# Optimization experiments

Measured on AMD Instinct MI355X. Metric: run time of the kernel, lower is better.

The kernel has to match this reference:

```python
import jax, jax.numpy as jnp
import numpy as np
import math

B, C, SEG, SEGLEN, K, GROUPS, WG = 8, 256, 40, 200, 10, 32, 4
L4 = SEGLEN // 4            # 50 temporal slots per segment
N = SEG * L4                # 2000 total points
WIDTH = GROUPS * WG         # 128 bottleneck width


def build_neighbor_idx(seg_lens):
    """Exact numpy replication of torch get_temporal_graph's neighbor-list loop.
    Returns flat (into B*N rows) neighbor indices of shape (B, N, 3)."""
    seg_lens = np.asarray(seg_lens)
    Bn, S = seg_lens.shape
    nb = np.zeros((Bn, S * L4, 3), dtype=np.int64)
    for i in range(Bn):
        last_valid = 0
        skip_seg = 0
        base = i * S * L4
        for j in range(S):
            valid = math.ceil(seg_lens[i, j] / 4.0)
            for k in range(L4):
                idx = j * L4 + k
                if k < valid:
                    nb[i, idx] = [base + last_valid, base + idx, base + idx]
                    last_valid = idx
                    if k == 0 and j != 0:
                        nb[i, skip_seg, 2] = base + idx
                    if k == valid - 1:
                        skip_seg = idx
                    else:
                        nb[i, idx, 2] = base + idx + 1
                else:
                    nb[i, idx] = [base + idx] * 3
    return nb


def conv1x1(x, W, b):
    # x: (B, Cin, N, T), W: (Cout, Cin)
    return jnp.einsum('bcnt,oc->bont', x, W) + b[None, :, None, None]


def grouped_1x3(x, W, b):
    # x: (B, WIDTH, N, 3), W: (WIDTH, WIDTH//GROUPS, 3); valid conv -> T_out = 1
    Bn, _, Nn, _ = x.shape
    xg = x.reshape(Bn, GROUPS, WIDTH // GROUPS, Nn, 3)
    Wg = W.reshape(GROUPS, WIDTH // GROUPS, WIDTH // GROUPS, 3)
    y = jnp.einsum('bgcnt,goct->bgon', xg, Wg)
    return y.reshape(Bn, WIDTH, Nn, 1) + b[None, :, None, None]


def grouped_1x1(x, W, b):
    # x: (B, WIDTH, N, T), W: (WIDTH, WIDTH//GROUPS)
    Bn, _, Nn, T = x.shape
    xg = x.reshape(Bn, GROUPS, WIDTH // GROUPS, Nn, T)
    Wg = W.reshape(GROUPS, WIDTH // GROUPS, WIDTH // GROUPS)
    y = jnp.einsum('bgcnt,goc->bgont', xg, Wg)
    return y.reshape(Bn, WIDTH, Nn, T) + b[None, :, None, None]


def setup_inputs() -> dict:
    key = jax.random.key(0)
    ks = jax.random.split(key, 10)
    s = 0.05
    x = jax.random.normal(ks[0], (B, C, N), dtype=jnp.float32)
    seg_lens = jax.random.randint(ks[1], (B, SEG), 0, 201)
    neighbor_idx = jnp.asarray(build_neighbor_idx(np.asarray(seg_lens)))
    return dict(
        x=x, seg_lens=seg_lens, neighbor_idx=neighbor_idx,
        tW1=jax.random.normal(ks[2], (WIDTH, C), jnp.float32) * s,
        tb1=jnp.zeros((WIDTH,), jnp.float32),
        tW2=jax.random.normal(ks[3], (WIDTH, WIDTH // GROUPS, 3), jnp.float32) * s,
        tb2=jnp.zeros((WIDTH,), jnp.float32),
        tW3=jax.random.normal(ks[4], (C, WIDTH), jnp.float32) * s,
        tb3=jnp.zeros((C,), jnp.float32),
        sW1=jax.random.normal(ks[5], (WIDTH, 2 * C), jnp.float32) * s,
        sb1=jnp.zeros((WIDTH,), jnp.float32),
        sW2=jax.random.normal(ks[6], (WIDTH, WIDTH // GROUPS), jnp.float32) * s,
        sb2=jnp.zeros((WIDTH,), jnp.float32),
        sW3=jax.random.normal(ks[7], (C, WIDTH), jnp.float32) * s,
        sb3=jnp.zeros((C,), jnp.float32),
    )


def reference(x, seg_lens, neighbor_idx, tW1, tb1, tW2, tb2, tW3, tb3,
              sW1, sb1, sW2, sb2, sW3, sb3):
    relu = jax.nn.relu
    B_, C_, N_ = x.shape
    flat = x.transpose(0, 2, 1).reshape(B_ * N_, C_)  # (B*N, C)

    # --- temporal branch: gather 3 temporal-graph neighbors -> (B, C, N, 3) ---
    tg = flat[neighbor_idx.reshape(-1)].reshape(B_, N_, 3, C_).transpose(0, 3, 1, 2)
    h = relu(conv1x1(tg, tW1, tb1))
    h = relu(grouped_1x3(h, tW2, tb2))
    tout = conv1x1(h, tW3, tb3).max(axis=-1)  # (B, C, N)

    # --- semantic branch: kNN graph feature (style=1) ---
    xx = jnp.sum(x * x, axis=1)                       # (B, N)
    inner = jnp.einsum('bci,bcj->bij', x, x)          # (B, N, N)
    pd = 2.0 * inner - xx[:, None, :] - xx[:, :, None]  # negative sq. distances
    _, idx = jax.lax.top_k(pd, K)                     # (B, N, K)
    base = (jnp.arange(B_) * N_)[:, None, None]
    nbr = flat[(idx + base).reshape(-1)].reshape(B_, N_, K, C_)
    center = jnp.broadcast_to(x.transpose(0, 2, 1)[:, :, None, :], (B_, N_, K, C_))
    xf = jnp.concatenate([nbr, center], axis=3).transpose(0, 3, 1, 2)  # (B, 2C, N, K)
    g = relu(conv1x1(xf, sW1, sb1))
    g = relu(grouped_1x1(g, sW2, sb2))
    sout = conv1x1(g, sW3, sb3).max(axis=-1)  # (B, C, N)

    return relu(tout + x + sout)
```

## Files before the change

kernel.cpp:

```cpp
#include <hip/hip_runtime.h>

#define NPTS 2000
#define NBATCH 8
#define NC 256
#define NW 128
#define NK 10
#define NROWS (NBATCH * NPTS)
#define JPAD 2048

typedef _Float16 f16x8 __attribute__((ext_vector_type(8)));
typedef _Float16 f16x4 __attribute__((ext_vector_type(4)));
typedef float f32x4 __attribute__((ext_vector_type(4)));

__device__ __forceinline__ float dot4(float4 a, float4 b) {
    return a.x*b.x + a.y*b.y + a.z*b.z + a.w*b.w;
}
__device__ __forceinline__ float4 relu4(float4 a) {
    return make_float4(fmaxf(a.x,0.f), fmaxf(a.y,0.f), fmaxf(a.z,0.f), fmaxf(a.w,0.f));
}
__device__ __forceinline__ float4 add4(float4 a, float4 b) {
    return make_float4(a.x+b.x, a.y+b.y, a.z+b.z, a.w+b.w);
}

__device__ __forceinline__ void ins10(float d, int j, float* vals, int* idxs) {
    if (d > vals[9]) {
        float v = d; int id = j;
        #pragma unroll
        for (int s = 0; s < 10; ++s) {
            if (v > vals[s]) {
                float tv = vals[s]; vals[s] = v; v = tv;
                int   ti = idxs[s]; idxs[s] = id; id = ti;
            }
        }
    }
}

__device__ __forceinline__ void gl_lds16(const void* g, void* l) {
    __builtin_amdgcn_global_load_lds(
        (const __attribute__((address_space(1))) void*)g,
        (__attribute__((address_space(3))) void*)l, 16, 0, 0);
}

__global__ __launch_bounds__(256) void k_prep(
    const float* __restrict__ x, _Float16* __restrict__ xb,
    float* __restrict__ xx)
{
    __shared__ float T[64][259];
    __shared__ float Pp[64][4];
    const int t  = threadIdx.x;
    const int b  = blockIdx.x >> 5;
    const int n0 = (blockIdx.x & 31) * 64;

    #pragma unroll
    for (int p = 0; p < 64; ++p) {
        const int idx = p*256 + t;
        const int c = idx >> 6, nl = idx & 63;
        T[nl][c] = x[((size_t)b*NC + c)*NPTS + min(n0 + nl, NPTS-1)];
    }
    __syncthreads();

    const int row = t & 63, q = t >> 6;
    const int gr  = n0 + row;
    const bool ok = gr < NPTS;
    const int sx  = gr & 7;
    float ss = 0.f;
    #pragma unroll
    for (int u = 0; u < 2; ++u) {
        const int kc = 2*q + u;
        const size_t base = ((size_t)(b*8 + kc)*JPAD + gr) * 64;
        #pragma unroll
        for (int g = 0; g < 4; ++g) {
            f16x8 vh, vl;
            #pragma unroll
            for (int e = 0; e < 8; ++e) {
                const float f = ok ? T[row][kc*32 + g*8 + e] : 0.f;
                ss = fmaf(f, f, ss);
                const _Float16 h = (_Float16)f;
                vh[e] = h;
                vl[e] = (_Float16)(f - (float)h);
            }
            *(f16x8*)&xb[base + (size_t)((g     ^ sx))*8] = vh;
            *(f16x8*)&xb[base + (size_t)(((4|g) ^ sx))*8] = vl;
        }
    }
    Pp[row][q] = ss;
    __syncthreads();
    if (t < 64 && n0 + t < NPTS)
        xx[(size_t)b*NPTS + n0 + t] = Pp[t][0] + Pp[t][1] + Pp[t][2] + Pp[t][3];
}

__global__ __launch_bounds__(256) void k_wprep(const float* __restrict__ a,
                                               _Float16* __restrict__ o, int n)
{
    const int i = (blockIdx.x*256 + threadIdx.x)*4;
    if (i < n) {
        const float4 v = *(const float4*)&a[i];
        f16x4 h = {(_Float16)v.x, (_Float16)v.y, (_Float16)v.z, (_Float16)v.w};
        *(f16x4*)&o[i] = h;
    }
}

__global__ __launch_bounds__(256) void k_wcat(
    const float* __restrict__ tW1, const float* __restrict__ sW1,
    _Float16* __restrict__ whcat)
{
    const int idx = blockIdx.x*256 + threadIdx.x;
    const int n = idx >> 8, k = idx & 255;
    float v;
    if (n < 128)      v = tW1[n*256 + k];
    else if (n < 256) v = sW1[(n-128)*512 + k];
    else              v = sW1[(n-256)*512 + 256 + k];
    whcat[idx] = (_Float16)v;
}

__global__ __launch_bounds__(256) void k_rowmm(
    const _Float16* __restrict__ xb, const _Float16* __restrict__ whcat,
    const float* __restrict__ tb1, const float* __restrict__ sb1,
    float* __restrict__ T1r, float* __restrict__ P, float* __restrict__ Q)
{
    const int t = threadIdx.x, lane = t & 63, w = t >> 6;
    const int lr = lane & 15, rg = lane >> 4;
    const int r0 = blockIdx.x * 16;
    const int b  = r0 / NPTS, jr = r0 % NPTS;

    const int row = jr + lr;
    const int sx  = row & 7;
    f16x8 ah[8], al[8];
    #pragma unroll
    for (int kc = 0; kc < 8; ++kc) {
        const size_t base = ((size_t)(b*8 + kc)*JPAD + row) * 64;
        ah[kc] = *(const f16x8*)&xb[base + (size_t)((rg     ^ sx))*8];
        al[kc] = *(const f16x8*)&xb[base + (size_t)(((4|rg) ^ sx))*8];
    }

    #pragma unroll
    for (int nt = 0; nt < 6; ++nt) {
        const int n0 = (w*6 + nt) * 16;
        f32x4 acc = {0.f,0.f,0.f,0.f};
        #pragma unroll
        for (int kc = 0; kc < 8; ++kc) {
            const f16x8 bw = *(const f16x8*)&whcat[(size_t)(n0 + lr)*256 + kc*32 + rg*8];
            acc = __builtin_amdgcn_mfma_f32_16x16x32_f16(ah[kc], bw, acc, 0,0,0);
            acc = __builtin_amdgcn_mfma_f32_16x16x32_f16(al[kc], bw, acc, 0,0,0);
        }
        const int n = n0 + lr;
        float bias; bool dorelu; float* dst;
        if (n < 128)      { bias = tb1[n];     dorelu = true;  dst = T1r + (size_t)r0*NW + n; }
        else if (n < 256) { bias = 0.f;        dorelu = false; dst = P   + (size_t)r0*NW + (n-128); }
        else              { bias = sb1[n-256]; dorelu = false; dst = Q   + (size_t)r0*NW + (n-256); }
        #pragma unroll
        for (int q = 0; q < 4; ++q) {
            float v = acc[q] + bias;
            if (dorelu) v = fmaxf(v, 0.f);
            dst[(size_t)(rg*4 + q)*NW] = v;
        }
    }
}

__global__ __launch_bounds__(256, 2) void k_topk(
    const _Float16* __restrict__ xb, const float* __restrict__ xx,
    float* __restrict__ pval, int* __restrict__ pidx)
{
    __shared__ __align__(16) char smem[65536];

    const int t    = threadIdx.x;
    const int b    = blockIdx.x & 7;
    const int ip   = (blockIdx.x >> 3) & 15;
    const int j4   = blockIdx.x >> 7;
    const int i0   = ip * 128;
    const int lane = t & 63;
    const int w    = t >> 6;
    const int lr   = lane & 15, rg = lane >> 4;
    const char* xbb = (const char*)xb;
    const float* xxb = xx + (size_t)b * NPTS;

    f32x4 acc[2][8] = {};
    float v0[10], v1[10]; int x0[10], x1[10];
    #pragma unroll
    for (int s = 0; s < 10; ++s) { v0[s]=v1[s]=-3.0e38f; x0[s]=x1[s]=0x7fffffff; }

    {
        const size_t gbase = (size_t)(b*8 + 0) * JPAD;
        const char* gi = xbb + (gbase + i0) * 128;
        const char* gj = xbb + (gbase + (size_t)(j4*4 + 0)*128) * 128;
        #pragma unroll
        for (int r2 = 0; r2 < 4; ++r2) {
            gl_lds16(gi + t*16 + r2*4096, smem + t*16 + r2*4096);
            gl_lds16(gj + t*16 + r2*4096, smem + 16384 + t*16 + r2*4096);
        }
    }
    __syncthreads();

    for (int step = 0; step < 32; ++step) {
        const int kc = step & 7, buf = step & 1, panel = step >> 3;

        if (step < 31) {
            const int ns = step + 1, nkc = ns & 7, npan = ns >> 3;
            const size_t gbase = (size_t)(b*8 + nkc) * JPAD;
            const char* gi = xbb + (gbase + i0) * 128;
            const char* gj = xbb + (gbase + (size_t)(j4*4 + npan)*128) * 128;
            char* li = smem + (buf ^ 1)*32768;
            #pragma unroll
            for (int r2 = 0; r2 < 4; ++r2) {
                gl_lds16(gi + t*16 + r2*4096, li + t*16 + r2*4096);
                gl_lds16(gj + t*16 + r2*4096, li + 16384 + t*16 + r2*4096);
            }
        }

        {
            const char* IB = smem + buf*32768;
            const char* JB = IB + 16384;
            f16x8 bhf[2], blf[2];
            #pragma unroll
            for (int it = 0; it < 2; ++it) {
                const int il = (w*2 + it)*16 + lr;
                const int sx = il & 7;
                bhf[it] = *(const f16x8*)(IB + il*128 + ((rg     ^ sx))*16);
                blf[it] = *(const f16x8*)(IB + il*128 + (((4|rg) ^ sx))*16);
            }
            #pragma unroll
            for (int jt = 0; jt < 8; ++jt) {
                const int jl = jt*16 + lr;
                const int sx = jl & 7;
                const f16x8 ajh = *(const f16x8*)(JB + jl*128 + ((rg     ^ sx))*16);
                const f16x8 ajl = *(const f16x8*)(JB + jl*128 + (((4|rg) ^ sx))*16);
                #pragma unroll
                for (int it = 0; it < 2; ++it) {
                    acc[it][jt] = __builtin_amdgcn_mfma_f32_16x16x32_f16(ajh, bhf[it], acc[it][jt], 0,0,0);
                    acc[it][jt] = __builtin_amdgcn_mfma_f32_16x16x32_f16(ajh, blf[it], acc[it][jt], 0,0,0);
                    acc[it][jt] = __builtin_amdgcn_mfma_f32_16x16x32_f16(ajl, bhf[it], acc[it][jt], 0,0,0);
                }
            }
        }

        if (kc == 7) {
            const int jpan = (j4*4 + panel)*128;
            #pragma unroll
            for (int jt = 0; jt < 8; ++jt) {
                const int jg0 = jpan + jt*16 + rg*4;
                const f32x4 xv = *(const f32x4*)&xxb[min(jg0, NPTS-4)];
                {
                    const float d0 = 2.f*acc[0][jt][0] - xv[0];
                    const float d1 = 2.f*acc[0][jt][1] - xv[1];
                    const float d2 = 2.f*acc[0][jt][2] - xv[2];
                    const float d3 = 2.f*acc[0][jt][3] - xv[3];
                    if (fmaxf(fmaxf(d0,d1), fmaxf(d2,d3)) > v0[9]) {
                        if (jg0     < NPTS) ins10(d0, jg0,     v0, x0);
                        if (jg0 + 1 < NPTS) ins10(d1, jg0 + 1, v0, x0);
                        if (jg0 + 2 < NPTS) ins10(d2, jg0 + 2, v0, x0);
                        if (jg0 + 3 < NPTS) ins10(d3, jg0 + 3, v0, x0);
                    }
                    acc[0][jt] = (f32x4){0.f,0.f,0.f,0.f};
                }
                {
                    const float d0 = 2.f*acc[1][jt][0] - xv[0];
                    const float d1 = 2.f*acc[1][jt][1] - xv[1];
                    const float d2 = 2.f*acc[1][jt][2] - xv[2];
                    const float d3 = 2.f*acc[1][jt][3] - xv[3];
                    if (fmaxf(fmaxf(d0,d1), fmaxf(d2,d3)) > v1[9]) {
                        if (jg0     < NPTS) ins10(d0, jg0,     v1, x1);
                        if (jg0 + 1 < NPTS) ins10(d1, jg0 + 1, v1, x1);
                        if (jg0 + 2 < NPTS) ins10(d2, jg0 + 2, v1, x1);
                        if (jg0 + 3 < NPTS) ins10(d3, jg0 + 3, v1, x1);
                    }
                    acc[1][jt] = (f32x4){0.f,0.f,0.f,0.f};
                }
            }
        }
        __syncthreads();
    }

    float* mval = (float*)smem;
    int*   midx = (int*)(smem + 20480);
    {
        const int g0 = (w*2 + 0)*16 + lr;
        const int g1 = (w*2 + 1)*16 + lr;
        #pragma unroll
        for (int s = 0; s < 10; ++s) {
            mval[(g0*4 + rg)*10 + s] = v0[s];  midx[(g0*4 + rg)*10 + s] = x0[s];
            mval[(g1*4 + rg)*10 + s] = v1[s];  midx[(g1*4 + rg)*10 + s] = x1[s];
        }
    }
    __syncthreads();
    {
        const int g = t >> 1, pr = t & 1;
        float* va = &mval[(g*4 + pr)*10];     int* ia = &midx[(g*4 + pr)*10];
        const float* vb = &mval[(g*4 + pr + 2)*10]; const int* ib = &midx[(g*4 + pr + 2)*10];
        float ov[10]; int oi[10]; int pa = 0, pb = 0;
        #pragma unroll
        for (int s = 0; s < 10; ++s) {
            const float A = va[pa], Bv = vb[pb];
            const int  Ai = ia[pa], Bi = ib[pb];
            const bool ta = (A > Bv) || (A == Bv && Ai < Bi);
            ov[s] = ta ? A : Bv; oi[s] = ta ? Ai : Bi;
            pa += ta ? 1 : 0; pb += ta ? 0 : 1;
        }
        #pragma unroll
        for (int s = 0; s < 10; ++s) { va[s] = ov[s]; ia[s] = oi[s]; }
    }
    __syncthreads();
    if (t < 128) {
        const int g = t;
        const int ig = i0 + g;
        if (ig < NPTS) {
            const float* va = &mval[(g*4 + 0)*10]; const int* ia = &midx[(g*4 + 0)*10];
            const float* vb = &mval[(g*4 + 1)*10]; const int* ib = &midx[(g*4 + 1)*10];
            float* ov = &pval[((size_t)(b*NPTS + ig)*4 + j4)*10];
            int*   oi = &pidx[((size_t)(b*NPTS + ig)*4 + j4)*10];
            int pa = 0, pb = 0;
            #pragma unroll
            for (int s = 0; s < 10; ++s) {
                const float A = va[pa], Bv = vb[pb];
                const int  Ai = ia[pa], Bi = ib[pb];
                const bool ta = (A > Bv) || (A == Bv && Ai < Bi);
                ov[s] = ta ? A : Bv; oi[s] = ta ? Ai : Bi;
                pa += ta ? 1 : 0; pb += ta ? 0 : 1;
            }
        }
    }
}

__global__ __launch_bounds__(256) void k_tkmerge(
    const float* __restrict__ pval, const int* __restrict__ pidx,
    int* __restrict__ tk)
{
    const int r = blockIdx.x*256 + threadIdx.x;
    if (r >= NROWS) return;
    const float* v  = &pval[(size_t)r*40];
    const int*   ix = &pidx[(size_t)r*40];
    const int base = (r / NPTS) * NPTS;
    int* op = &tk[(size_t)r*NK];
    int p0 = 0, p1 = 0, p2 = 0, p3 = 0;
    #pragma unroll
    for (int s = 0; s < NK; ++s) {
        float bv = -3.4e38f; int bi = 0x7fffffff; int bl = 0;
        {
            const float vv = v[p0];       const int ii = ix[p0];
            if (vv > bv || (vv == bv && ii < bi)) { bv = vv; bi = ii; bl = 0; }
        }
        {
            const float vv = v[10 + p1];  const int ii = ix[10 + p1];
            if (vv > bv || (vv == bv && ii < bi)) { bv = vv; bi = ii; bl = 1; }
        }
        {
            const float vv = v[20 + p2];  const int ii = ix[20 + p2];
            if (vv > bv || (vv == bv && ii < bi)) { bv = vv; bi = ii; bl = 2; }
        }
        {
            const float vv = v[30 + p3];  const int ii = ix[30 + p3];
            if (vv > bv || (vv == bv && ii < bi)) { bv = vv; bi = ii; bl = 3; }
        }
        p0 += (bl == 0); p1 += (bl == 1); p2 += (bl == 2); p3 += (bl == 3);
        op[s] = base + bi;
    }
}

#define AST 136
__global__ __launch_bounds__(256, 2) void k_fused(
    const float* __restrict__ x,
    const int* __restrict__ nb, const int* __restrict__ tk,
    const float* __restrict__ T1r, const float* __restrict__ P, const float* __restrict__ Q,
    const float* __restrict__ tW2, const float* __restrict__ tb2,
    const float* __restrict__ sW2, const float* __restrict__ sb2,
    const _Float16* __restrict__ wt3h, const _Float16* __restrict__ ws3h,
    const float* __restrict__ tb3, const float* __restrict__ sb3,
    float* __restrict__ out)
{
    __shared__ __align__(16) _Float16 A16[144*AST];
    __shared__ float Ssm[8][260];
    __shared__ float Zr[8][260];

    const int t  = threadIdx.x;
    const int r0 = blockIdx.x * 8;
    const int bb = r0 / NPTS;
    const int n0 = r0 % NPTS;

    {
        const float4 z4 = make_float4(0.f,0.f,0.f,0.f);
        float4* p4 = (float4*)A16;
        #pragma unroll
        for (int i = 0; i < 10; ++i) {
            const int idx = t + i*256;
            if (idx < 2448) p4[idx] = z4;
        }
    }
    __syncthreads();

    {
        const int o    = t & 127;
        const int half = t >> 7;
        const int g4   = o & ~3;

        const float4 f0 = *(const float4*)&tW2[o*12];
        const float4 f1 = *(const float4*)&tW2[o*12 + 4];
        const float4 f2 = *(const float4*)&tW2[o*12 + 8];
        const float4 wt0 = make_float4(f0.x, f0.w, f1.z, f2.y);
        const float4 wt1 = make_float4(f0.y, f1.x, f1.w, f2.z);
        const float4 wt2 = make_float4(f0.z, f1.y, f2.x, f2.w);
        const float4 wsw = *(const float4*)&sW2[o*4];
        const float tb2o = tb2[o], sb2o = sb2[o];

        #pragma unroll
        for (int ptl = 0; ptl < 4; ++ptl) {
            const int pt = half*4 + ptl;
            const int r  = r0 + pt;
            const int nb0 = nb[r*3+0], nb1 = nb[r*3+1], nb2 = nb[r*3+2];
            int ki[NK];
            #pragma unroll
            for (int k = 0; k < NK; ++k) ki[k] = tk[r*NK + k];
            const float4 h0 = *(const float4*)&T1r[(size_t)nb0*NW + g4];
            const float4 h1 = *(const float4*)&T1r[(size_t)nb1*NW + g4];
            const float4 h2 = *(const float4*)&T1r[(size_t)nb2*NW + g4];
            const float4 qf = *(const float4*)&Q[(size_t)r*NW + g4];
            float4 pf[NK];
            #pragma unroll
            for (int k = 0; k < NK; ++k) pf[k] = *(const float4*)&P[(size_t)ki[k]*NW + g4];

            const float z = tb2o + dot4(wt0,h0) + dot4(wt1,h1) + dot4(wt2,h2);
            A16[(128 + pt)*AST + o] = (_Float16)fmaxf(z, 0.f);
            #pragma unroll
            for (int k = 0; k < NK; ++k) {
                const float4 g1 = relu4(add4(pf[k], qf));
                A16[(pt*16 + k)*AST + o] = (_Float16)fmaxf(dot4(wsw, g1) + sb2o, 0.f);
            }
        }
    }
    __syncthreads();

    const int lane = t & 63, w = t >> 6;
    const int lr = lane & 15, lg = lane >> 4;
    const int n0w = w * 64;

    f32x4 accG[8][4] = {};
    f32x4 accZ[4] = {};

    #pragma unroll
    for (int kt = 0; kt < 4; ++kt) {
        const int ko = kt*32 + lg*8;
        f16x8 bs[4], bt[4];
        #pragma unroll
        for (int nt = 0; nt < 4; ++nt) {
            const int n = n0w + nt*16 + lr;
            bs[nt] = *(const f16x8*)&ws3h[n*NW + ko];
            bt[nt] = *(const f16x8*)&wt3h[n*NW + ko];
        }
        #pragma unroll
        for (int mt = 0; mt < 8; ++mt) {
            const f16x8 a = *(const f16x8*)&A16[(mt*16 + lr)*AST + ko];
            #pragma unroll
            for (int nt = 0; nt < 4; ++nt)
                accG[mt][nt] = __builtin_amdgcn_mfma_f32_16x16x32_f16(a, bs[nt], accG[mt][nt], 0,0,0);
        }
        const f16x8 az = *(const f16x8*)&A16[(128 + lr)*AST + ko];
        #pragma unroll
        for (int nt = 0; nt < 4; ++nt)
            accZ[nt] = __builtin_amdgcn_mfma_f32_16x16x32_f16(az, bt[nt], accZ[nt], 0,0,0);
    }

    const int rg = lg;
    #pragma unroll
    for (int mt = 0; mt < 8; ++mt) {
        #pragma unroll
        for (int nt = 0; nt < 4; ++nt) {
            float v;
            if (rg < 2)       v = fmaxf(fmaxf(accG[mt][nt][0], accG[mt][nt][1]),
                                        fmaxf(accG[mt][nt][2], accG[mt][nt][3]));
            else if (rg == 2) v = fmaxf(accG[mt][nt][0], accG[mt][nt][1]);
            else              v = -3.0e38f;
            v = fmaxf(v, __shfl_xor(v, 16));
            v = fmaxf(v, __shfl_xor(v, 32));
            if (lane < 16) Ssm[mt][n0w + nt*16 + lane] = v;
        }
    }
    #pragma unroll
    for (int nt = 0; nt < 4; ++nt) {
        #pragma unroll
        for (int q = 0; q < 4; ++q) {
            if (rg < 2) Zr[rg*4 + q][n0w + nt*16 + lr] = accZ[nt][q];
        }
    }
    __syncthreads();

    {
        const int c = t;
        const float tb = tb3[c], sb = sb3[c];
        const size_t go = ((size_t)bb*NC + c)*NPTS + n0;
        const float4 xv0 = *(const float4*)&x[go];
        const float4 xv1 = *(const float4*)&x[go + 4];
        const float xr[8] = {xv0.x,xv0.y,xv0.z,xv0.w, xv1.x,xv1.y,xv1.z,xv1.w};
        float ov[8];
        #pragma unroll
        for (int p = 0; p < 8; ++p)
            ov[p] = fmaxf(Zr[p][c] + tb + Ssm[p][c] + sb + xr[p], 0.f);
        *(float4*)&out[go]     = make_float4(ov[0],ov[1],ov[2],ov[3]);
        *(float4*)&out[go + 4] = make_float4(ov[4],ov[5],ov[6],ov[7]);
    }
}

extern "C" void kernel_launch(void* const* d_in, const int* in_sizes, int n_in,
                              void* d_out, int out_size, void* d_ws, size_t ws_size,
                              hipStream_t stream) {
    (void)in_sizes; (void)n_in; (void)out_size; (void)ws_size;
    const float* x   = (const float*)d_in[0];
    const int*   nb  = (const int*)d_in[2];
    const float* tW1 = (const float*)d_in[3];
    const float* tb1 = (const float*)d_in[4];
    const float* tW2 = (const float*)d_in[5];
    const float* tb2 = (const float*)d_in[6];
    const float* tW3 = (const float*)d_in[7];
    const float* tb3 = (const float*)d_in[8];
    const float* sW1 = (const float*)d_in[9];
    const float* sb1 = (const float*)d_in[10];
    const float* sW2 = (const float*)d_in[11];
    const float* sb2 = (const float*)d_in[12];
    const float* sW3 = (const float*)d_in[13];
    const float* sb3 = (const float*)d_in[14];
    float* out = (float*)d_out;

    float* ws  = (float*)d_ws;
    float* T1r  = ws;
    float* P    = ws + 2048000;
    float* Q    = ws + 4096000;
    float* xxp  = ws + 6144000;
    int*   tk   = (int*)(ws + 6160000);
    float* pval = ws + 6320000;
    int*   pidx = (int*)(ws + 6960000);
    _Float16* xb    = (_Float16*)(ws + 7600000);
    _Float16* whcat = xb + (size_t)NBATCH * 8 * JPAD * 64;
    _Float16* wt3h  = whcat + 384 * 256;
    _Float16* ws3h  = wt3h + NC * NW;

    k_prep<<<NBATCH * 32, 256, 0, stream>>>(x, xb, xxp);
    k_wcat<<<384, 256, 0, stream>>>(tW1, sW1, whcat);
    k_wprep<<<32, 256, 0, stream>>>(tW3, wt3h, NC * NW);
    k_wprep<<<32, 256, 0, stream>>>(sW3, ws3h, NC * NW);
    k_rowmm<<<NROWS / 16, 256, 0, stream>>>(xb, whcat, tb1, sb1, T1r, P, Q);
    k_topk<<<512, 256, 0, stream>>>(xb, xxp, pval, pidx);
    k_tkmerge<<<(NROWS + 255) / 256, 256, 0, stream>>>(pval, pidx, tk);
    k_fused<<<NROWS / 8, 256, 0, stream>>>(x, nb, tk, T1r, P, Q,
                                           tW2, tb2, sW2, sb2, wt3h, ws3h, tb3, sb3, out);
}
```

Measured before the change: 372.4 us.

## Split kNN distance tiles across more blocks and add two-level top-k merge

The distance/top-k kernel now handles one 128-column j panel per block instead of four, so the grid grows from 512 to 2048 blocks and each block does a single partial top-10 pass at the end. Each row then has 16 partial lists, which are merged in two stages (4→1 then 4→1) through new workspace buffers. The goal is more parallelism and occupancy on the GPU for the dominant distance GEMM. The cost is reloading the i tile four times as often, more partial-result traffic, and one extra kernel launch.

```diff
diff --git a/kernel.cpp b/kernel.cpp
--- a/kernel.cpp
+++ b/kernel.cpp
@@ -157,17 +157,18 @@
     }
 }
 
-__global__ __launch_bounds__(256, 2) void k_topk(
-    const _Float16* __restrict__ xb, const float* __restrict__ xx,
-    float* __restrict__ pval, int* __restrict__ pidx)
+__global__ __attribute__((amdgpu_flat_work_group_size(256,256), amdgpu_waves_per_eu(2,2)))
+void k_dist(const _Float16* __restrict__ xb, const float* __restrict__ xx,
+            float* __restrict__ pval, int* __restrict__ pidx)
 {
     __shared__ __align__(16) char smem[65536];
 
     const int t    = threadIdx.x;
     const int b    = blockIdx.x & 7;
     const int ip   = (blockIdx.x >> 3) & 15;
-    const int j4   = blockIdx.x >> 7;
+    const int jp   = blockIdx.x >> 7;
     const int i0   = ip * 128;
+    const int j0p  = jp * 128;
     const int lane = t & 63;
     const int w    = t >> 6;
     const int lr   = lane & 15, rg = lane >> 4;
@@ -175,14 +176,11 @@
     const float* xxb = xx + (size_t)b * NPTS;
 
     f32x4 acc[2][8] = {};
-    float v0[10], v1[10]; int x0[10], x1[10];
-    #pragma unroll
-    for (int s = 0; s < 10; ++s) { v0[s]=v1[s]=-3.0e38f; x0[s]=x1[s]=0x7fffffff; }
 
     {
         const size_t gbase = (size_t)(b*8 + 0) * JPAD;
         const char* gi = xbb + (gbase + i0) * 128;
-        const char* gj = xbb + (gbase + (size_t)(j4*4 + 0)*128) * 128;
+        const char* gj = xbb + (gbase + j0p) * 128;
         #pragma unroll
         for (int r2 = 0; r2 < 4; ++r2) {
             gl_lds16(gi + t*16 + r2*4096, smem + t*16 + r2*4096);
@@ -191,14 +189,13 @@
     }
     __syncthreads();
 
-    for (int step = 0; step < 32; ++step) {
-        const int kc = step & 7, buf = step & 1, panel = step >> 3;
-
-        if (step < 31) {
-            const int ns = step + 1, nkc = ns & 7, npan = ns >> 3;
-            const size_t gbase = (size_t)(b*8 + nkc) * JPAD;
+    for (int kc = 0; kc < 8; ++kc) {
+        const int buf = kc & 1;
+
+        if (kc < 7) {
+            const size_t gbase = (size_t)(b*8 + kc + 1) * JPAD;
             const char* gi = xbb + (gbase + i0) * 128;
-            const char* gj = xbb + (gbase + (size_t)(j4*4 + npan)*128) * 128;
+            const char* gj = xbb + (gbase + j0p) * 128;
             char* li = smem + (buf ^ 1)*32768;
             #pragma unroll
             for (int r2 = 0; r2 < 4; ++r2) {
@@ -232,42 +229,41 @@
                 }
             }
         }
-
-        if (kc == 7) {
-            const int jpan = (j4*4 + panel)*128;
-            #pragma unroll
-            for (int jt = 0; jt < 8; ++jt) {
-                const int jg0 = jpan + jt*16 + rg*4;
-                const f32x4 xv = *(const f32x4*)&xxb[min(jg0, NPTS-4)];
-                {
-                    const float d0 = 2.f*acc[0][jt][0] - xv[0];
-                    const float d1 = 2.f*acc[0][jt][1] - xv[1];
-                    const float d2 = 2.f*acc[0][jt][2] - xv[2];
-                    const float d3 = 2.f*acc[0][jt][3] - xv[3];
-                    if (fmaxf(fmaxf(d0,d1), fmaxf(d2,d3)) > v0[9]) {
-                        if (jg0     < NPTS) ins10(d0, jg0,     v0, x0);
-                        if (jg0 + 1 < NPTS) ins10(d1, jg0 + 1, v0, x0);
-                        if (jg0 + 2 < NPTS) ins10(d2, jg0 + 2, v0, x0);
-                        if (jg0 + 3 < NPTS) ins10(d3, jg0 + 3, v0, x0);
-                    }
-                    acc[0][jt] = (f32x4){0.f,0.f,0.f,0.f};
-                }
-                {
-                    const float d0 = 2.f*acc[1][jt][0] - xv[0];
-                    const float d1 = 2.f*acc[1][jt][1] - xv[1];
-                    const float d2 = 2.f*acc[1][jt][2] - xv[2];
-                    const float d3 = 2.f*acc[1][jt][3] - xv[3];
-                    if (fmaxf(fmaxf(d0,d1), fmaxf(d2,d3)) > v1[9]) {
-                        if (jg0     < NPTS) ins10(d0, jg0,     v1, x1);
-                        if (jg0 + 1 < NPTS) ins10(d1, jg0 + 1, v1, x1);
-                        if (jg0 + 2 < NPTS) ins10(d2, jg0 + 2, v1, x1);
-                        if (jg0 + 3 < NPTS) ins10(d3, jg0 + 3, v1, x1);
-                    }
-                    acc[1][jt] = (f32x4){0.f,0.f,0.f,0.f};
-                }
-            }
-        }
         __syncthreads();
+    }
+
+    float v0[10], v1[10]; int x0[10], x1[10];
+    #pragma unroll
+    for (int s = 0; s < 10; ++s) { v0[s]=v1[s]=-3.0e38f; x0[s]=x1[s]=0x7fffffff; }
+
+    #pragma unroll
+    for (int jt = 0; jt < 8; ++jt) {
+        const int jg0 = j0p + jt*16 + rg*4;
+        const f32x4 xv = *(const f32x4*)&xxb[min(jg0, NPTS-4)];
+        {
+            const float d0 = 2.f*acc[0][jt][0] - xv[0];
+            const float d1 = 2.f*acc[0][jt][1] - xv[1];
+            const float d2 = 2.f*acc[0][jt][2] - xv[2];
+            const float d3 = 2.f*acc[0][jt][3] - xv[3];
+            if (fmaxf(fmaxf(d0,d1), fmaxf(d2,d3)) > v0[9]) {
+                if (jg0     < NPTS) ins10(d0, jg0,     v0, x0);
+                if (jg0 + 1 < NPTS) ins10(d1, jg0 + 1, v0, x0);
+                if (jg0 + 2 < NPTS) ins10(d2, jg0 + 2, v0, x0);
+                if (jg0 + 3 < NPTS) ins10(d3, jg0 + 3, v0, x0);
+            }
+        }
+        {
+            const float d0 = 2.f*acc[1][jt][0] - xv[0];
+            const float d1 = 2.f*acc[1][jt][1] - xv[1];
+            const float d2 = 2.f*acc[1][jt][2] - xv[2];
+            const float d3 = 2.f*acc[1][jt][3] - xv[3];
+            if (fmaxf(fmaxf(d0,d1), fmaxf(d2,d3)) > v1[9]) {
+                if (jg0     < NPTS) ins10(d0, jg0,     v1, x1);
+                if (jg0 + 1 < NPTS) ins10(d1, jg0 + 1, v1, x1);
+                if (jg0 + 2 < NPTS) ins10(d2, jg0 + 2, v1, x1);
+                if (jg0 + 3 < NPTS) ins10(d3, jg0 + 3, v1, x1);
+            }
+        }
     }
 
     float* mval = (float*)smem;
@@ -305,8 +301,8 @@
         if (ig < NPTS) {
             const float* va = &mval[(g*4 + 0)*10]; const int* ia = &midx[(g*4 + 0)*10];
             const float* vb = &mval[(g*4 + 1)*10]; const int* ib = &midx[(g*4 + 1)*10];
-            float* ov = &pval[((size_t)(b*NPTS + ig)*4 + j4)*10];
-            int*   oi = &pidx[((size_t)(b*NPTS + ig)*4 + j4)*10];
+            float* ov = &pval[((size_t)(b*NPTS + ig)*16 + jp)*10];
+            int*   oi = &pidx[((size_t)(b*NPTS + ig)*16 + jp)*10];
             int pa = 0, pb = 0;
             #pragma unroll
             for (int s = 0; s < 10; ++s) {
@@ -320,36 +316,56 @@
     }
 }
 
-__global__ __launch_bounds__(256) void k_tkmerge(
+__global__ __launch_bounds__(256) void k_tkm1(
     const float* __restrict__ pval, const int* __restrict__ pidx,
+    float* __restrict__ pval2, int* __restrict__ pidx2)
+{
+    const int idx = blockIdx.x*256 + threadIdx.x;
+    if (idx >= NROWS*4) return;
+    const int r = idx >> 2, qt = idx & 3;
+    const float* v  = &pval[((size_t)r*16 + qt*4)*10];
+    const int*   ix = &pidx[((size_t)r*16 + qt*4)*10];
+    float* ov = &pval2[(size_t)idx*10];
+    int*   oi = &pidx2[(size_t)idx*10];
+    int p0 = 0, p1 = 0, p2 = 0, p3 = 0;
+    #pragma unroll
+    for (int s = 0; s < NK; ++s) {
+        float bv = -3.4e38f; int bi = 0x7fffffff; int bl = 0;
+        { const float vv = v[p0];      const int ii = ix[p0];
+          if (vv > bv || (vv == bv && ii < bi)) { bv = vv; bi = ii; bl = 0; } }
+        { const float vv = v[10 + p1]; const int ii = ix[10 + p1];
+          if (vv > bv || (vv == bv && ii < bi)) { bv = vv; bi = ii; bl = 1; } }
+        { const float vv = v[20 + p2]; const int ii = ix[20 + p2];
+          if (vv > bv || (vv == bv && ii < bi)) { bv = vv; bi = ii; bl = 2; } }
+        { const float vv = v[30 + p3]; const int ii = ix[30 + p3];
+          if (vv > bv || (vv == bv && ii < bi)) { bv = vv; bi = ii; bl = 3; } }
+        p0 += (bl == 0); p1 += (bl == 1); p2 += (bl == 2); p3 += (bl == 3);
+        ov[s] = bv; oi[s] = bi;
+    }
+}
+
+__global__ __launch_bounds__(256) void k_tkm2(
+    const float* __restrict__ pval2, const int* __restrict__ pidx2,
     int* __restrict__ tk)
 {
     const int r = blockIdx.x*256 + threadIdx.x;
     if (r >= NROWS) return;
-    const float* v  = &pval[(size_t)r*40];
-    const int*   ix = &pidx[(size_t)r*40];
+    const float* v  = &pval2[(size_t)r*40];
+    const int*   ix = &pidx2[(size_t)r*40];
     const int base = (r / NPTS) * NPTS;
     int* op = &tk[(size_t)r*NK];
     int p0 = 0, p1 = 0, p2 = 0, p3 = 0;
     #pragma unroll
     for (int s = 0; s < NK; ++s) {
         float bv = -3.4e38f; int bi = 0x7fffffff; int bl = 0;
-        {
-            const float vv = v[p0];       const int ii = ix[p0];
-            if (vv > bv || (vv == bv && ii < bi)) { bv = vv; bi = ii; bl = 0; }
-        }
-        {
-            const float vv = v[10 + p1];  const int ii = ix[10 + p1];
-            if (vv > bv || (vv == bv && ii < bi)) { bv = vv; bi = ii; bl = 1; }
-        }
-        {
-            const float vv = v[20 + p2];  const int ii = ix[20 + p2];
-            if (vv > bv || (vv == bv && ii < bi)) { bv = vv; bi = ii; bl = 2; }
-        }
-        {
-            const float vv = v[30 + p3];  const int ii = ix[30 + p3];
-            if (vv > bv || (vv == bv && ii < bi)) { bv = vv; bi = ii; bl = 3; }
-        }
+        { const float vv = v[p0];      const int ii = ix[p0];
+          if (vv > bv || (vv == bv && ii < bi)) { bv = vv; bi = ii; bl = 0; } }
+        { const float vv = v[10 + p1]; const int ii = ix[10 + p1];
+          if (vv > bv || (vv == bv && ii < bi)) { bv = vv; bi = ii; bl = 1; } }
+        { const float vv = v[20 + p2]; const int ii = ix[20 + p2];
+          if (vv > bv || (vv == bv && ii < bi)) { bv = vv; bi = ii; bl = 2; } }
+        { const float vv = v[30 + p3]; const int ii = ix[30 + p3];
+          if (vv > bv || (vv == bv && ii < bi)) { bv = vv; bi = ii; bl = 3; } }
         p0 += (bl == 0); p1 += (bl == 1); p2 += (bl == 2); p3 += (bl == 3);
         op[s] = base + bi;
     }
@@ -518,14 +534,16 @@
     float* out = (float*)d_out;
 
     float* ws  = (float*)d_ws;
-    float* T1r  = ws;
-    float* P    = ws + 2048000;
-    float* Q    = ws + 4096000;
-    float* xxp  = ws + 6144000;
-    int*   tk   = (int*)(ws + 6160000);
-    float* pval = ws + 6320000;
-    int*   pidx = (int*)(ws + 6960000);
-    _Float16* xb    = (_Float16*)(ws + 7600000);
+    float* T1r   = ws;
+    float* P     = ws + 2048000;
+    float* Q     = ws + 4096000;
+    float* xxp   = ws + 6144000;
+    int*   tk    = (int*)(ws + 6160000);
+    float* pval  = ws + 6320000;
+    int*   pidx  = (int*)(ws + 8880000);
+    float* pval2 = ws + 11440000;
+    int*   pidx2 = (int*)(ws + 12080000);
+    _Float16* xb    = (_Float16*)(ws + 12720000);
     _Float16* whcat = xb + (size_t)NBATCH * 8 * JPAD * 64;
     _Float16* wt3h  = whcat + 384 * 256;
     _Float16* ws3h  = wt3h + NC * NW;
@@ -535,8 +553,9 @@
     k_wprep<<<32, 256, 0, stream>>>(tW3, wt3h, NC * NW);
     k_wprep<<<32, 256, 0, stream>>>(sW3, ws3h, NC * NW);
     k_rowmm<<<NROWS / 16, 256, 0, stream>>>(xb, whcat, tb1, sb1, T1r, P, Q);
-    k_topk<<<512, 256, 0, stream>>>(xb, xxp, pval, pidx);
-    k_tkmerge<<<(NROWS + 255) / 256, 256, 0, stream>>>(pval, pidx, tk);
+    k_dist<<<2048, 256, 0, stream>>>(xb, xxp, pval, pidx);
+    k_tkm1<<<(NROWS*4 + 255) / 256, 256, 0, stream>>>(pval, pidx, pval2, pidx2);
+    k_tkm2<<<(NROWS + 255) / 256, 256, 0, stream>>>(pval2, pidx2, tk);
     k_fused<<<NROWS / 8, 256, 0, stream>>>(x, nb, tk, T1r, P, Q,
                                            tW2, tb2, sW2, sb2, wt3h, ws3h, tb3, sb3, out);
 }
```

Measured after the change: 390.9 us. 5.0% more time.
